# Kernel tuning notes

Hardware: AMD Instinct MI355X
Metric: run time of the kernel (lower is better)

## Reference

```python
import jax, jax.numpy as jnp
import numpy as np

B, N, D, H = 2, 1024, 1024, 16
DH = D // H
SCALE = 1.0 / DH ** 0.5
STJ_Q = 1.0
NUM_ITER = 4
CAUSAL = True
EPS = 1e-6


def setup_inputs() -> dict:
    key = jax.random.key(0)
    k1, k2, k3 = jax.random.split(key, 3)
    x = jax.random.normal(k1, (B, N, D), jnp.float32)
    Wqkv = jax.random.normal(k2, (3 * D, D), jnp.float32) / np.float32(np.sqrt(D))
    Wo = jax.random.normal(k3, (D, D), jnp.float32) / np.float32(np.sqrt(D))
    return {"x": x, "Wqkv": Wqkv, "Wo": Wo}


def stieltjes_attention(Q, K, V, scale, causal, q, num_iter):
    # Q,K,V: [B,H,N,dh]. Scores s: [B,H,N,N].
    n = Q.shape[2]
    s = jnp.einsum('bhnd,bhmd->bhnm', Q, K) * scale
    if causal:
        mask = jnp.tril(jnp.ones((n, n), bool))  # [N,N], True = attend
    else:
        mask = jnp.ones((n, n), bool)
    # Solve per-row lambda s.t. sum_j (lambda - s_j)^(-q) = 1 (Stieltjes-transform
    # normalization) with Newton iterations; masked entries contribute 0.
    s_masked = jnp.where(mask, s, -1e30)
    lam = s_masked.max(-1) + 1.0  # [B,H,N], start above max score
    for _ in range(num_iter):
        d = jnp.maximum(lam[..., None] - s, EPS)  # [B,H,N,N]
        w = jnp.where(mask, d ** (-q), 0.0)
        f = w.sum(-1) - 1.0
        fp = -q * jnp.where(mask, d ** (-q - 1.0), 0.0).sum(-1)
        lam = lam - f / fp
    d = jnp.maximum(lam[..., None] - s, EPS)
    p = jnp.where(mask, d ** (-q), 0.0)
    p = p / p.sum(-1, keepdims=True)  # final exact normalization
    return jnp.einsum('bhnm,bhmd->bhnd', p, V)


def reference(x, Wqkv, Wo):
    b, n, dmodel = x.shape
    qkv = (x @ Wqkv.T).reshape(b, n, 3, H, DH).transpose(2, 0, 3, 1, 4)
    Q, K, V = qkv[0], qkv[1], qkv[2]
    o = stieltjes_attention(Q, K, V, SCALE, CAUSAL, STJ_Q, NUM_ITER)
    o = o.transpose(0, 2, 1, 3).reshape(b, n, dmodel)
    return o @ Wo.T
```

## Files before the change

kernel.cpp:

```cpp
#include <hip/hip_runtime.h>
#include <hip/hip_bf16.h>
#include <math.h>

#define HNUM 16
#define DH 64
#define NSEQ 1024
#define BATCH 2
#define DMODEL 1024
#define SCALE 0.125f
#define EPS 1e-6f
#define NUM_ITER 4
#define SPAD 1048

typedef float f32x4 __attribute__((ext_vector_type(4)));
typedef short bfrag __attribute__((ext_vector_type(8)));
typedef unsigned int u32x4 __attribute__((ext_vector_type(4)));

__device__ inline float bf2f_u(unsigned int u) {
    return __builtin_bit_cast(float, u << 16);
}
__device__ inline unsigned short f2bf_u(float f) {
    return __builtin_bit_cast(unsigned short, __float2bfloat16(f));
}

__device__ inline void gload16(const __hip_bfloat16* g, __hip_bfloat16* l) {
    __builtin_amdgcn_global_load_lds(
        (const __attribute__((address_space(1))) void*)g,
        (__attribute__((address_space(3))) void*)l, 16, 0, 0);
}

__global__ __launch_bounds__(256) void cast3(const float* __restrict__ s0, __hip_bfloat16* __restrict__ d0, int n0,
                                             const float* __restrict__ s1, __hip_bfloat16* __restrict__ d1, int n1,
                                             const float* __restrict__ s2, __hip_bfloat16* __restrict__ d2, int n2) {
    const int stride = gridDim.x * blockDim.x;
    const int tot = n0 + n1 + n2;
    for (int i = blockIdx.x * blockDim.x + threadIdx.x; i < tot; i += stride) {
        const float* s; __hip_bfloat16* d; int off;
        if (i < n0)            { s = s0; d = d0; off = i; }
        else if (i < n0 + n1)  { s = s1; d = d1; off = i - n0; }
        else                   { s = s2; d = d2; off = i - n0 - n1; }
        const float4 v = *reinterpret_cast<const float4*>(&s[(size_t)off * 4]);
        ushort4 o;
        o.x = f2bf_u(v.x); o.y = f2bf_u(v.y); o.z = f2bf_u(v.z); o.w = f2bf_u(v.w);
        *reinterpret_cast<ushort4*>(&d[(size_t)off * 4]) = o;
    }
}

template <bool OUT_BF16>
__global__ __launch_bounds__(256) void gemm_bt(const __hip_bfloat16* __restrict__ A,
                                               const __hip_bfloat16* __restrict__ B,
                                               void* __restrict__ Cv,
                                               int M, int Nc, int K) {
    __shared__ __align__(16) __hip_bfloat16 As[64 * 64];
    __shared__ __align__(16) __hip_bfloat16 Bs[128 * 64];
    const int tid  = threadIdx.x;
    const int l    = tid & 63;
    const int wave = tid >> 6;
    const int m0 = blockIdx.y * 64, n0 = blockIdx.x * 128;
    const int wr = (wave >> 1) * 32, wc = (wave & 1) * 64;
    const int lr = l & 15;
    const int lk = (l >> 4) * 8;

    f32x4 acc[2][4];
#pragma unroll
    for (int m = 0; m < 2; ++m)
#pragma unroll
        for (int n = 0; n < 4; ++n) acc[m][n] = (f32x4){0.f, 0.f, 0.f, 0.f};

    for (int k0 = 0; k0 < K; k0 += 64) {
#pragma unroll
        for (int p = 0; p < 2; ++p) {
            const int idx = tid + p * 256;
            const int r = idx >> 3, ce = (idx & 7) * 8;
            gload16(&A[(size_t)(m0 + r) * K + k0 + ce], &As[idx * 8]);
        }
#pragma unroll
        for (int p = 0; p < 4; ++p) {
            const int idx = tid + p * 256;
            const int r = idx >> 3, ce = (idx & 7) * 8;
            gload16(&B[(size_t)(n0 + r) * K + k0 + ce], &Bs[idx * 8]);
        }
        __syncthreads();

#pragma unroll
        for (int kk = 0; kk < 64; kk += 32) {
            bfrag af[2], bfr[4];
#pragma unroll
            for (int m = 0; m < 2; ++m)
                af[m] = *reinterpret_cast<const bfrag*>(&As[(wr + m * 16 + lr) * 64 + kk + lk]);
#pragma unroll
            for (int n = 0; n < 4; ++n)
                bfr[n] = *reinterpret_cast<const bfrag*>(&Bs[(wc + n * 16 + lr) * 64 + kk + lk]);
#pragma unroll
            for (int m = 0; m < 2; ++m)
#pragma unroll
                for (int n = 0; n < 4; ++n)
                    acc[m][n] = __builtin_amdgcn_mfma_f32_16x16x32_bf16(
                        af[m], bfr[n], acc[m][n], 0, 0, 0);
        }
        __syncthreads();
    }

#pragma unroll
    for (int m = 0; m < 2; ++m) {
        const int row0 = m0 + wr + m * 16 + (l >> 4) * 4;
#pragma unroll
        for (int n = 0; n < 4; ++n) {
            const int col = n0 + wc + n * 16 + lr;
#pragma unroll
            for (int j = 0; j < 4; ++j) {
                if constexpr (OUT_BF16) {
                    ((__hip_bfloat16*)Cv)[(size_t)(row0 + j) * Nc + col] =
                        __float2bfloat16(acc[m][n][j]);
                } else {
                    ((float*)Cv)[(size_t)(row0 + j) * Nc + col] = acc[m][n][j];
                }
            }
        }
    }
}

__global__ __launch_bounds__(256) void transpose_v(const __hip_bfloat16* __restrict__ qkvb,
                                                   __hip_bfloat16* __restrict__ Vt) {
    const int bh = blockIdx.x >> 4;
    const int nc = blockIdx.x & 15;
    const int b = bh >> 4, h = bh & 15;
    __shared__ unsigned short tile[64][80];
    const int t = threadIdx.x;
    {
        const int r = t >> 2, cc = (t & 3) * 16;
        const size_t src = ((size_t)(b * NSEQ + nc * 64 + r)) * 3072 + 2048 + h * 64 + cc;
        const uint4 v0 = *reinterpret_cast<const uint4*>(&qkvb[src]);
        const uint4 v1 = *reinterpret_cast<const uint4*>(&qkvb[src + 8]);
        *reinterpret_cast<uint4*>(&tile[r][cc])     = v0;
        *reinterpret_cast<uint4*>(&tile[r][cc + 8]) = v1;
    }
    __syncthreads();
    {
        const int d = t >> 2, n2 = (t & 3) * 16;
        unsigned int e[16];
#pragma unroll
        for (int k = 0; k < 16; ++k) e[k] = tile[n2 + k][d];
        uint4 o0, o1;
        o0.x = e[0]  | (e[1]  << 16); o0.y = e[2]  | (e[3]  << 16);
        o0.z = e[4]  | (e[5]  << 16); o0.w = e[6]  | (e[7]  << 16);
        o1.x = e[8]  | (e[9]  << 16); o1.y = e[10] | (e[11] << 16);
        o1.z = e[12] | (e[13] << 16); o1.w = e[14] | (e[15] << 16);
        const size_t dst = ((size_t)(bh * 64 + d)) * 1024 + nc * 64 + n2;
        *reinterpret_cast<uint4*>(&Vt[dst])     = o0;
        *reinterpret_cast<uint4*>(&Vt[dst + 8]) = o1;
    }
}

template <int NQ>
__device__ inline void newton2_wb(unsigned short* __restrict__ SA,
                                  unsigned short* __restrict__ SB,
                                  int ncolsA, int ncolsB, int limit, int lane) {
    constexpr int NC = NQ * 2;
    float svA[NC * 2], svB[NC * 2];
#pragma unroll
    for (int t = 0; t < NC; ++t) {
        const int c = lane * 2 + t * 128;
        const unsigned int uA = *reinterpret_cast<const unsigned int*>(&SA[c]);
        const unsigned int uB = *reinterpret_cast<const unsigned int*>(&SB[c]);
        float a0 = bf2f_u(uA & 0xffffu), a1 = bf2f_u(uA >> 16);
        float b0 = bf2f_u(uB & 0xffffu), b1 = bf2f_u(uB >> 16);
        if (t >= NC - 2) {
            a0 = (c     < ncolsA) ? a0 : -1e30f;
            a1 = (c + 1 < ncolsA) ? a1 : -1e30f;
            b0 = (c     < ncolsB) ? b0 : -1e30f;
            b1 = (c + 1 < ncolsB) ? b1 : -1e30f;
        }
        svA[2 * t] = a0; svA[2 * t + 1] = a1;
        svB[2 * t] = b0; svB[2 * t + 1] = b1;
    }

    float mA = svA[0], mB = svB[0];
#pragma unroll
    for (int e = 1; e < 2 * NC; ++e) { mA = fmaxf(mA, svA[e]); mB = fmaxf(mB, svB[e]); }
#pragma unroll
    for (int off = 32; off; off >>= 1) {
        mA = fmaxf(mA, __shfl_xor(mA, off));
        mB = fmaxf(mB, __shfl_xor(mB, off));
    }
    float lamA = mA + 1.0f, lamB = mB + 1.0f;

    for (int it = 0; it < NUM_ITER; ++it) {
        float fA = 0.f, fpA = 0.f, fB = 0.f, fpB = 0.f;
#pragma unroll
        for (int e = 0; e < 2 * NC; ++e) {
            const float iA = __builtin_amdgcn_rcpf(fmaxf(lamA - svA[e], EPS));
            fA += iA; fpA = fmaf(iA, iA, fpA);
            const float iB = __builtin_amdgcn_rcpf(fmaxf(lamB - svB[e], EPS));
            fB += iB; fpB = fmaf(iB, iB, fpB);
        }
#pragma unroll
        for (int off = 32; off; off >>= 1) {
            fA += __shfl_xor(fA, off); fpA += __shfl_xor(fpA, off);
            fB += __shfl_xor(fB, off); fpB += __shfl_xor(fpB, off);
        }
        lamA += (fA - 1.0f) / fpA;
        lamB += (fB - 1.0f) / fpB;
    }

    float swA = 0.f, swB = 0.f;
#pragma unroll
    for (int e = 0; e < 2 * NC; ++e) {
        svA[e] = __builtin_amdgcn_rcpf(fmaxf(lamA - svA[e], EPS)); swA += svA[e];
        svB[e] = __builtin_amdgcn_rcpf(fmaxf(lamB - svB[e], EPS)); swB += svB[e];
    }
#pragma unroll
    for (int off = 32; off; off >>= 1) {
        swA += __shfl_xor(swA, off);
        swB += __shfl_xor(swB, off);
    }
    const float iswA = __builtin_amdgcn_rcpf(swA);
    const float iswB = __builtin_amdgcn_rcpf(swB);

#pragma unroll
    for (int t = 0; t < NC; ++t) {
        const int c = lane * 2 + t * 128;
        if (t * 128 < limit && c < limit) {
            const unsigned int pA = (unsigned)f2bf_u(svA[2 * t] * iswA)
                                  | ((unsigned)f2bf_u(svA[2 * t + 1] * iswA) << 16);
            *reinterpret_cast<unsigned int*>(&SA[c]) = pA;
            const unsigned int pB = (unsigned)f2bf_u(svB[2 * t] * iswB)
                                  | ((unsigned)f2bf_u(svB[2 * t + 1] * iswB) << 16);
            *reinterpret_cast<unsigned int*>(&SB[c]) = pB;
        }
    }
}

__global__ __launch_bounds__(512) void attn_mfma(const __hip_bfloat16* __restrict__ qkvb,
                                                 const __hip_bfloat16* __restrict__ Vt,
                                                 __hip_bfloat16* __restrict__ obf) {
    const int tid  = threadIdx.x;
    const int lane = tid & 63;
    const int wave = tid >> 6;
    const int qt = blockIdx.x & 63;
    const int bh = blockIdx.x >> 6;
    const int b = bh >> 4, h = bh & 15;
    const int r0 = qt * 16;

    __shared__ __align__(16) unsigned short S[16][SPAD];

    const size_t qbase = (size_t)(b * NSEQ) * 3072;
    const int lr  = lane & 15;
    const int lk8 = (lane >> 4) * 8;
    const int rj0 = (lane >> 4) * 4;

    const __hip_bfloat16* qrow = qkvb + qbase + (size_t)(r0 + lr) * 3072 + h * 64;
    const bfrag a0 = *reinterpret_cast<const bfrag*>(&qrow[lk8]);
    const bfrag a1 = *reinterpret_cast<const bfrag*>(&qrow[32 + lk8]);
    const __hip_bfloat16* kglob = qkvb + qbase + 1024 + h * 64;
    for (int jt = wave; jt <= qt + 1; jt += 8) {
        if (jt <= qt) {
            const int jrow = jt * 16 + lr;
            const bfrag b0 = *reinterpret_cast<const bfrag*>(&kglob[(size_t)jrow * 3072 + lk8]);
            const bfrag b1 = *reinterpret_cast<const bfrag*>(&kglob[(size_t)jrow * 3072 + 32 + lk8]);
            f32x4 c = (f32x4){0.f, 0.f, 0.f, 0.f};
            c = __builtin_amdgcn_mfma_f32_16x16x32_bf16(a0, b0, c, 0, 0, 0);
            c = __builtin_amdgcn_mfma_f32_16x16x32_bf16(a1, b1, c, 0, 0, 0);
#pragma unroll
            for (int j = 0; j < 4; ++j)
                S[rj0 + j][jt * 16 + lr] = f2bf_u(c[j] * SCALE);
        } else {
#pragma unroll
            for (int j = 0; j < 4; ++j)
                S[rj0 + j][jt * 16 + lr] = 0;
        }
    }
    __syncthreads();

    {
        const int rowA = wave * 2, rowB = rowA + 1;
        const int ncolsA = r0 + rowA + 1, ncolsB = r0 + rowB + 1;
        const int limit = r0 + 16;
        const int nq = (ncolsB + 255) >> 8;
        switch (nq) {
            case 1:  newton2_wb<1>(S[rowA], S[rowB], ncolsA, ncolsB, limit, lane); break;
            case 2:  newton2_wb<2>(S[rowA], S[rowB], ncolsA, ncolsB, limit, lane); break;
            case 3:  newton2_wb<3>(S[rowA], S[rowB], ncolsA, ncolsB, limit, lane); break;
            default: newton2_wb<4>(S[rowA], S[rowB], ncolsA, ncolsB, limit, lane); break;
        }
    }
    __syncthreads();

    if (wave < 4) {
        const int dt = wave;
        const __hip_bfloat16* vtrow = Vt + ((size_t)(bh * 64 + dt * 16 + lr)) * 1024;

        f32x4 acc0 = (f32x4){0.f, 0.f, 0.f, 0.f};
        f32x4 acc1 = (f32x4){0.f, 0.f, 0.f, 0.f};
        for (int j0 = 0; j0 <= r0; j0 += 64) {
            {
                const bfrag pa = *reinterpret_cast<const bfrag*>(&S[lr][j0 + lk8]);
                const bfrag pb = *reinterpret_cast<const bfrag*>(&vtrow[j0 + lk8]);
                acc0 = __builtin_amdgcn_mfma_f32_16x16x32_bf16(pa, pb, acc0, 0, 0, 0);
            }
            if (j0 + 32 <= r0) {
                const bfrag pa = *reinterpret_cast<const bfrag*>(&S[lr][j0 + 32 + lk8]);
                const bfrag pb = *reinterpret_cast<const bfrag*>(&vtrow[j0 + 32 + lk8]);
                acc1 = __builtin_amdgcn_mfma_f32_16x16x32_bf16(pa, pb, acc1, 0, 0, 0);
            }
        }

#pragma unroll
        for (int j = 0; j < 4; ++j) {
            const int row = rj0 + j;
            obf[(size_t)(b * NSEQ + r0 + row) * 1024 + h * 64 + dt * 16 + lr] =
                __float2bfloat16(acc0[j] + acc1[j]);
        }
    }
}

extern "C" void kernel_launch(void* const* d_in, const int* in_sizes, int n_in,
                              void* d_out, int out_size, void* d_ws, size_t ws_size,
                              hipStream_t stream) {
    const float* x    = (const float*)d_in[0];
    const float* Wqkv = (const float*)d_in[1];
    const float* Wo   = (const float*)d_in[2];
    float* out = (float*)d_out;

    const int M = BATCH * NSEQ;
    char* ws = (char*)d_ws;
    __hip_bfloat16* xbf  = (__hip_bfloat16*)ws; ws += (size_t)M * DMODEL * 2;
    __hip_bfloat16* wqbf = (__hip_bfloat16*)ws; ws += (size_t)3 * DMODEL * DMODEL * 2;
    __hip_bfloat16* wobf = (__hip_bfloat16*)ws; ws += (size_t)DMODEL * DMODEL * 2;
    __hip_bfloat16* qkvb = (__hip_bfloat16*)ws; ws += (size_t)M * 3 * DMODEL * 2;
    __hip_bfloat16* Vt   = (__hip_bfloat16*)ws; ws += (size_t)BATCH * HNUM * DH * NSEQ * 2;
    __hip_bfloat16* obf  = (__hip_bfloat16*)ws; ws += (size_t)M * DMODEL * 2;

    dim3 blk(256);
    cast3<<<2048, blk, 0, stream>>>(x, xbf, M * DMODEL / 4,
                                    Wqkv, wqbf, 3 * DMODEL * DMODEL / 4,
                                    Wo, wobf, DMODEL * DMODEL / 4);

    dim3 g1(3 * DMODEL / 128, M / 64);
    gemm_bt<true><<<g1, blk, 0, stream>>>(xbf, wqbf, qkvb, M, 3 * DMODEL, DMODEL);

    transpose_v<<<512, blk, 0, stream>>>(qkvb, Vt);

    attn_mfma<<<2048, dim3(512), 0, stream>>>(qkvb, Vt, obf);

    dim3 g2(DMODEL / 128, M / 64);
    gemm_bt<false><<<g2, blk, 0, stream>>>(obf, wobf, out, M, DMODEL, DMODEL);
}
```

Measured before the change: 122.1 us.

## Pair short and long causal query tiles per block for balanced attention work

Each attention block now handles two 16-row query tiles, tile p and tile 63-p, so every block does roughly the same causal work. The grid is halved. Both tiles' score rows sit side by side in a widened shared buffer, and all 8 waves do the PV MFMA instead of only 4. The Newton solver is templated separately on each row's column count, and masked tail loads are clamped so they do not read out of range. The cost is more shared memory per block, fewer blocks in flight, and extra select logic in the QK loop.

```diff
diff --git a/kernel.cpp b/kernel.cpp
--- a/kernel.cpp
+++ b/kernel.cpp
@@ -10,7 +10,7 @@
 #define SCALE 0.125f
 #define EPS 1e-6f
 #define NUM_ITER 4
-#define SPAD 1048
+#define SPAD_T 1080
 
 typedef float f32x4 __attribute__((ext_vector_type(4)));
 typedef short bfrag __attribute__((ext_vector_type(8)));
@@ -152,32 +152,45 @@
     }
 }
 
-template <int NQ>
+template <int NQA, int NQB>
 __device__ inline void newton2_wb(unsigned short* __restrict__ SA,
                                   unsigned short* __restrict__ SB,
-                                  int ncolsA, int ncolsB, int limit, int lane) {
-    constexpr int NC = NQ * 2;
-    float svA[NC * 2], svB[NC * 2];
-#pragma unroll
-    for (int t = 0; t < NC; ++t) {
+                                  int ncolsA, int ncolsB,
+                                  int limitA, int limitB, int lane) {
+    constexpr int NCA = NQA * 2, NCB = NQB * 2;
+    float svA[NCA * 2], svB[NCB * 2];
+#pragma unroll
+    for (int t = 0; t < NCA; ++t) {
         const int c = lane * 2 + t * 128;
-        const unsigned int uA = *reinterpret_cast<const unsigned int*>(&SA[c]);
-        const unsigned int uB = *reinterpret_cast<const unsigned int*>(&SB[c]);
-        float a0 = bf2f_u(uA & 0xffffu), a1 = bf2f_u(uA >> 16);
-        float b0 = bf2f_u(uB & 0xffffu), b1 = bf2f_u(uB >> 16);
-        if (t >= NC - 2) {
-            a0 = (c     < ncolsA) ? a0 : -1e30f;
-            a1 = (c + 1 < ncolsA) ? a1 : -1e30f;
-            b0 = (c     < ncolsB) ? b0 : -1e30f;
-            b1 = (c + 1 < ncolsB) ? b1 : -1e30f;
-        }
-        svA[2 * t] = a0; svA[2 * t + 1] = a1;
-        svB[2 * t] = b0; svB[2 * t + 1] = b1;
+        int ca = c;
+        if (t >= NCA - 2) ca = (c < ncolsA) ? c : 0;
+        const unsigned int u = *reinterpret_cast<const unsigned int*>(&SA[ca]);
+        float v0 = bf2f_u(u & 0xffffu), v1 = bf2f_u(u >> 16);
+        if (t >= NCA - 2) {
+            v0 = (c     < ncolsA) ? v0 : -1e30f;
+            v1 = (c + 1 < ncolsA) ? v1 : -1e30f;
+        }
+        svA[2 * t] = v0; svA[2 * t + 1] = v1;
+    }
+#pragma unroll
+    for (int t = 0; t < NCB; ++t) {
+        const int c = lane * 2 + t * 128;
+        int cbm = c;
+        if (t >= NCB - 2) cbm = (c < ncolsB) ? c : 0;
+        const unsigned int u = *reinterpret_cast<const unsigned int*>(&SB[cbm]);
+        float v0 = bf2f_u(u & 0xffffu), v1 = bf2f_u(u >> 16);
+        if (t >= NCB - 2) {
+            v0 = (c     < ncolsB) ? v0 : -1e30f;
+            v1 = (c + 1 < ncolsB) ? v1 : -1e30f;
+        }
+        svB[2 * t] = v0; svB[2 * t + 1] = v1;
     }
 
     float mA = svA[0], mB = svB[0];
 #pragma unroll
-    for (int e = 1; e < 2 * NC; ++e) { mA = fmaxf(mA, svA[e]); mB = fmaxf(mB, svB[e]); }
+    for (int e = 1; e < 2 * NCA; ++e) mA = fmaxf(mA, svA[e]);
+#pragma unroll
+    for (int e = 1; e < 2 * NCB; ++e) mB = fmaxf(mB, svB[e]);
 #pragma unroll
     for (int off = 32; off; off >>= 1) {
         mA = fmaxf(mA, __shfl_xor(mA, off));
@@ -188,9 +201,12 @@
     for (int it = 0; it < NUM_ITER; ++it) {
         float fA = 0.f, fpA = 0.f, fB = 0.f, fpB = 0.f;
 #pragma unroll
-        for (int e = 0; e < 2 * NC; ++e) {
+        for (int e = 0; e < 2 * NCA; ++e) {
             const float iA = __builtin_amdgcn_rcpf(fmaxf(lamA - svA[e], EPS));
             fA += iA; fpA = fmaf(iA, iA, fpA);
+        }
+#pragma unroll
+        for (int e = 0; e < 2 * NCB; ++e) {
             const float iB = __builtin_amdgcn_rcpf(fmaxf(lamB - svB[e], EPS));
             fB += iB; fpB = fmaf(iB, iB, fpB);
         }
@@ -205,8 +221,11 @@
 
     float swA = 0.f, swB = 0.f;
 #pragma unroll
-    for (int e = 0; e < 2 * NC; ++e) {
+    for (int e = 0; e < 2 * NCA; ++e) {
         svA[e] = __builtin_amdgcn_rcpf(fmaxf(lamA - svA[e], EPS)); swA += svA[e];
+    }
+#pragma unroll
+    for (int e = 0; e < 2 * NCB; ++e) {
         svB[e] = __builtin_amdgcn_rcpf(fmaxf(lamB - svB[e], EPS)); swB += svB[e];
     }
 #pragma unroll
@@ -218,15 +237,21 @@
     const float iswB = __builtin_amdgcn_rcpf(swB);
 
 #pragma unroll
-    for (int t = 0; t < NC; ++t) {
+    for (int t = 0; t < NCA; ++t) {
         const int c = lane * 2 + t * 128;
-        if (t * 128 < limit && c < limit) {
-            const unsigned int pA = (unsigned)f2bf_u(svA[2 * t] * iswA)
+        if (t * 128 < limitA && c < limitA) {
+            const unsigned int pk = (unsigned)f2bf_u(svA[2 * t] * iswA)
                                   | ((unsigned)f2bf_u(svA[2 * t + 1] * iswA) << 16);
-            *reinterpret_cast<unsigned int*>(&SA[c]) = pA;
-            const unsigned int pB = (unsigned)f2bf_u(svB[2 * t] * iswB)
+            *reinterpret_cast<unsigned int*>(&SA[c]) = pk;
+        }
+    }
+#pragma unroll
+    for (int t = 0; t < NCB; ++t) {
+        const int c = lane * 2 + t * 128;
+        if (t * 128 < limitB && c < limitB) {
+            const unsigned int pk = (unsigned)f2bf_u(svB[2 * t] * iswB)
                                   | ((unsigned)f2bf_u(svB[2 * t + 1] * iswB) << 16);
-            *reinterpret_cast<unsigned int*>(&SB[c]) = pB;
+            *reinterpret_cast<unsigned int*>(&SB[c]) = pk;
         }
     }
 }
@@ -237,69 +262,83 @@
     const int tid  = threadIdx.x;
     const int lane = tid & 63;
     const int wave = tid >> 6;
-    const int qt = blockIdx.x & 63;
-    const int bh = blockIdx.x >> 6;
+    const int pair = blockIdx.x & 31;
+    const int bh = blockIdx.x >> 5;
     const int b = bh >> 4, h = bh & 15;
-    const int r0 = qt * 16;
-
-    __shared__ __align__(16) unsigned short S[16][SPAD];
+    const int qtA = pair, qtB = 63 - pair;
+    const int r0A = qtA * 16, r0B = qtB * 16;
+    const int sbBase = r0A + 32;
+
+    __shared__ __align__(16) unsigned short S[16][SPAD_T];
 
     const size_t qbase = (size_t)(b * NSEQ) * 3072;
     const int lr  = lane & 15;
     const int lk8 = (lane >> 4) * 8;
     const int rj0 = (lane >> 4) * 4;
 
-    const __hip_bfloat16* qrow = qkvb + qbase + (size_t)(r0 + lr) * 3072 + h * 64;
-    const bfrag a0 = *reinterpret_cast<const bfrag*>(&qrow[lk8]);
-    const bfrag a1 = *reinterpret_cast<const bfrag*>(&qrow[32 + lk8]);
+    const __hip_bfloat16* qrowA = qkvb + qbase + (size_t)(r0A + lr) * 3072 + h * 64;
+    const __hip_bfloat16* qrowB = qkvb + qbase + (size_t)(r0B + lr) * 3072 + h * 64;
+    const bfrag aA0 = *reinterpret_cast<const bfrag*>(&qrowA[lk8]);
+    const bfrag aA1 = *reinterpret_cast<const bfrag*>(&qrowA[32 + lk8]);
+    const bfrag aB0 = *reinterpret_cast<const bfrag*>(&qrowB[lk8]);
+    const bfrag aB1 = *reinterpret_cast<const bfrag*>(&qrowB[32 + lk8]);
     const __hip_bfloat16* kglob = qkvb + qbase + 1024 + h * 64;
-    for (int jt = wave; jt <= qt + 1; jt += 8) {
-        if (jt <= qt) {
+
+    const int ntA = qtA + 2, ntB = qtB + 2;
+    for (int t = wave; t < ntA + ntB; t += 8) {
+        const bool isA = (t < ntA);
+        const int jt  = isA ? t : (t - ntA);
+        const int qtX = isA ? qtA : qtB;
+        const int cb  = isA ? 0 : sbBase;
+        if (jt <= qtX) {
             const int jrow = jt * 16 + lr;
             const bfrag b0 = *reinterpret_cast<const bfrag*>(&kglob[(size_t)jrow * 3072 + lk8]);
             const bfrag b1 = *reinterpret_cast<const bfrag*>(&kglob[(size_t)jrow * 3072 + 32 + lk8]);
             f32x4 c = (f32x4){0.f, 0.f, 0.f, 0.f};
-            c = __builtin_amdgcn_mfma_f32_16x16x32_bf16(a0, b0, c, 0, 0, 0);
-            c = __builtin_amdgcn_mfma_f32_16x16x32_bf16(a1, b1, c, 0, 0, 0);
+            c = __builtin_amdgcn_mfma_f32_16x16x32_bf16(isA ? aA0 : aB0, b0, c, 0, 0, 0);
+            c = __builtin_amdgcn_mfma_f32_16x16x32_bf16(isA ? aA1 : aB1, b1, c, 0, 0, 0);
 #pragma unroll
             for (int j = 0; j < 4; ++j)
-                S[rj0 + j][jt * 16 + lr] = f2bf_u(c[j] * SCALE);
+                S[rj0 + j][cb + jt * 16 + lr] = f2bf_u(c[j] * SCALE);
         } else {
 #pragma unroll
             for (int j = 0; j < 4; ++j)
-                S[rj0 + j][jt * 16 + lr] = 0;
+                S[rj0 + j][cb + jt * 16 + lr] = 0;
         }
     }
     __syncthreads();
 
     {
-        const int rowA = wave * 2, rowB = rowA + 1;
-        const int ncolsA = r0 + rowA + 1, ncolsB = r0 + rowB + 1;
-        const int limit = r0 + 16;
-        const int nq = (ncolsB + 255) >> 8;
-        switch (nq) {
-            case 1:  newton2_wb<1>(S[rowA], S[rowB], ncolsA, ncolsB, limit, lane); break;
-            case 2:  newton2_wb<2>(S[rowA], S[rowB], ncolsA, ncolsB, limit, lane); break;
-            case 3:  newton2_wb<3>(S[rowA], S[rowB], ncolsA, ncolsB, limit, lane); break;
-            default: newton2_wb<4>(S[rowA], S[rowB], ncolsA, ncolsB, limit, lane); break;
+        const int limitA = r0A + 16, limitB = r0B + 16;
+        for (int p = 0; p < 2; ++p) {
+            const int row = wave * 2 + p;
+            const int ncolsA = r0A + row + 1, ncolsB = r0B + row + 1;
+            if (qtA < 16)
+                newton2_wb<1, 4>(&S[row][0], &S[row][sbBase],
+                                 ncolsA, ncolsB, limitA, limitB, lane);
+            else
+                newton2_wb<2, 3>(&S[row][0], &S[row][sbBase],
+                                 ncolsA, ncolsB, limitA, limitB, lane);
         }
     }
     __syncthreads();
 
-    if (wave < 4) {
-        const int dt = wave;
+    {
+        const int tile = wave >> 2, dt = wave & 3;
+        const int r0t = tile ? r0B : r0A;
+        const int cb  = tile ? sbBase : 0;
         const __hip_bfloat16* vtrow = Vt + ((size_t)(bh * 64 + dt * 16 + lr)) * 1024;
 
         f32x4 acc0 = (f32x4){0.f, 0.f, 0.f, 0.f};
         f32x4 acc1 = (f32x4){0.f, 0.f, 0.f, 0.f};
-        for (int j0 = 0; j0 <= r0; j0 += 64) {
+        for (int j0 = 0; j0 <= r0t; j0 += 64) {
             {
-                const bfrag pa = *reinterpret_cast<const bfrag*>(&S[lr][j0 + lk8]);
+                const bfrag pa = *reinterpret_cast<const bfrag*>(&S[lr][cb + j0 + lk8]);
                 const bfrag pb = *reinterpret_cast<const bfrag*>(&vtrow[j0 + lk8]);
                 acc0 = __builtin_amdgcn_mfma_f32_16x16x32_bf16(pa, pb, acc0, 0, 0, 0);
             }
-            if (j0 + 32 <= r0) {
-                const bfrag pa = *reinterpret_cast<const bfrag*>(&S[lr][j0 + 32 + lk8]);
+            if (j0 + 32 <= r0t) {
+                const bfrag pa = *reinterpret_cast<const bfrag*>(&S[lr][cb + j0 + 32 + lk8]);
                 const bfrag pb = *reinterpret_cast<const bfrag*>(&vtrow[j0 + 32 + lk8]);
                 acc1 = __builtin_amdgcn_mfma_f32_16x16x32_bf16(pa, pb, acc1, 0, 0, 0);
             }
@@ -308,7 +347,7 @@
 #pragma unroll
         for (int j = 0; j < 4; ++j) {
             const int row = rj0 + j;
-            obf[(size_t)(b * NSEQ + r0 + row) * 1024 + h * 64 + dt * 16 + lr] =
+            obf[(size_t)(b * NSEQ + r0t + row) * 1024 + h * 64 + dt * 16 + lr] =
                 __float2bfloat16(acc0[j] + acc1[j]);
         }
     }
@@ -341,7 +380,7 @@
 
     transpose_v<<<512, blk, 0, stream>>>(qkvb, Vt);
 
-    attn_mfma<<<2048, dim3(512), 0, stream>>>(qkvb, Vt, obf);
+    attn_mfma<<<1024, dim3(512), 0, stream>>>(qkvb, Vt, obf);
 
     dim3 g2(DMODEL / 128, M / 64);
     gemm_bt<false><<<g2, blk, 0, stream>>>(obf, wobf, out, M, DMODEL, DMODEL);
```

Measured after the change: 115.4 us. 1.06x faster.
